# Performance work log

Hardware: AMD Instinct MI355X
Metric: run time of the kernel (lower is better)

Reference implementation:

```python
import jax, jax.numpy as jnp
import numpy as np

B, L, D, N = 4, 8192, 128, 32


def setup_inputs() -> dict:
    key = jax.random.key(0)
    ks = jax.random.split(key, 12)
    s = 0.05  # small init scale for stability of exp/cumsum
    return {
        "x": jax.random.normal(ks[0], (B, L, D), jnp.float32),
        "h_t_minus_1": jax.random.normal(ks[1], (B, L, D), jnp.float32),
        "A_log": jax.random.normal(ks[2], (D, N), jnp.float32),
        "D_param": jnp.ones((D,), jnp.float32),
        "W_x": jax.random.normal(ks[3], (D, 2 * N + D), jnp.float32) * s,
        "W_dt": jax.random.normal(ks[4], (D, D), jnp.float32) * s,
        "b_dt": jnp.zeros((D,), jnp.float32),
        "conv_w": jax.random.normal(ks[5], (3, D, D), jnp.float32) * s,  # (width, in, out)
        "conv_b": jnp.zeros((D,), jnp.float32),
        "W_f": jax.random.normal(ks[6], (D, D), jnp.float32) * s,
        "b_f": jnp.zeros((D,), jnp.float32),
    }


def reference(x, h_t_minus_1, A_log, D_param, W_x, W_dt, b_dt, conv_w, conv_b, W_f, b_f):
    d, n = A_log.shape
    A = -jnp.exp(A_log)  # (d, n)
    x_dbl = x @ W_x  # (b, l, d + 2n)
    delta, Bm, Cm = jnp.split(x_dbl, [d, d + n], axis=-1)
    delta = jax.nn.softplus(delta @ W_dt + b_dt)  # (b, l, d)

    # selective scan
    dA = jnp.einsum('bld,dn->bldn', delta, A)
    dB_u = jnp.einsum('bld,bld,bln->bldn', delta, h_t_minus_1, Bm)
    dA_cumsum = jnp.exp(jnp.cumsum(dA, axis=1) - dA)  # exclusive cumsum
    h_t = jnp.einsum('bldn,bln->bld', dB_u * dA_cumsum, Cm)
    h_t = h_t + h_t * D_param

    ssm_output = jax.nn.relu(h_t @ W_f + b_f)
    # causal Conv1D, kernel=3: left-pad by 2
    conv = jax.lax.conv_general_dilated(
        ssm_output, conv_w, window_strides=(1,), padding=[(2, 0)],
        dimension_numbers=('NWC', 'WIO', 'NWC')) + conv_b
    causal_output = jax.nn.relu(conv)
    fused_output = ssm_output * causal_output
    return (fused_output, h_t)
```

## Files before the change

### kernel.cpp

```cpp
#include <hip/hip_runtime.h>
#include <math.h>

typedef unsigned short ushort_t;
typedef __attribute__((ext_vector_type(8))) short short8v;
typedef __attribute__((ext_vector_type(4))) float f32x4;

constexpr int B_  = 4;
constexpr int L_  = 8192;
constexpr int D_  = 128;
constexpr int N_  = 32;
constexpr int BL  = B_ * L_;
constexpr int CH  = 32;
constexpr int NC  = L_ / CH;

__device__ inline unsigned bfr(float x) {
    unsigned u = __float_as_uint(x);
    return (u + 0x7fffu + ((u >> 16) & 1u)) >> 16;
}
__device__ inline unsigned pkbf(float a, float b) {
    return bfr(a) | (bfr(b) << 16);
}

__global__ __launch_bounds__(256) void prep(
    const float* __restrict__ Wx, const float* __restrict__ Wdt,
    const float* __restrict__ Wf, const float* __restrict__ Wconv,
    const float* __restrict__ A_log,
    ushort_t* __restrict__ Wt0, ushort_t* __restrict__ Wt1,
    ushort_t* __restrict__ Wt2, ushort_t* __restrict__ Wtc,
    float* __restrict__ negA)
{
    const int which = blockIdx.y;
    const int t = blockIdx.x * 256 + threadIdx.x;
    if (which == 6) {
        if (t < D_ * N_) negA[t] = -expf(A_log[t]);
        return;
    }
    const float* src; ushort_t* dst; int N;
    switch (which) {
        case 0: src = Wx;  dst = Wt0; N = 192; break;
        case 1: src = Wdt; dst = Wt1; N = 128; break;
        case 2: src = Wf;  dst = Wt2; N = 128; break;
        default:
            src = Wconv + (size_t)(which - 3) * 128 * 128;
            dst = Wtc  + (size_t)(which - 3) * 128 * 128;
            N = 128; break;
    }
    if (t >= N * 32) return;
    const int n = t >> 5, k4 = (t & 31) * 4;
    const float a0 = src[(size_t)(k4 + 0) * N + n];
    const float a1 = src[(size_t)(k4 + 1) * N + n];
    const float a2 = src[(size_t)(k4 + 2) * N + n];
    const float a3 = src[(size_t)(k4 + 3) * N + n];
    uint2 p; p.x = pkbf(a0, a1); p.y = pkbf(a2, a3);
    *reinterpret_cast<uint2*>(&dst[(size_t)n * 128 + k4]) = p;
}

template <int NCOLS, int MODE>
__global__ __launch_bounds__(256) void gemm_mfma(
    const float* __restrict__ Ag, const ushort_t* __restrict__ Wt,
    const float* __restrict__ bias,
    float* __restrict__ C0, float* __restrict__ C1, float* __restrict__ C2)
{
    __shared__ __align__(16) ushort_t Alds[64 * 64];
    __shared__ __align__(16) ushort_t Blds[NCOLS * 64];

    const int tid  = threadIdx.x;
    const int r0   = blockIdx.x * 64;
    const int wid  = tid >> 6, lane = tid & 63;
    const int wm   = wid >> 1, wn = wid & 1;
    const int lr   = lane & 15, kg = lane >> 4;
    constexpr int NF = NCOLS / 32;

    f32x4 acc[2][NF] = {};

    for (int kt = 0; kt < 128; kt += 64) {
        #pragma unroll
        for (int j = 0; j < 2; ++j) {
            const int g = tid + j * 256;
            const int row = g >> 3, k8 = (g & 7) * 8;
            const float* src = &Ag[(size_t)(r0 + row) * 128 + kt + k8];
            const float4 v0 = *reinterpret_cast<const float4*>(src);
            const float4 v1 = *reinterpret_cast<const float4*>(src + 4);
            uint4 p;
            p.x = pkbf(v0.x, v0.y); p.y = pkbf(v0.z, v0.w);
            p.z = pkbf(v1.x, v1.y); p.w = pkbf(v1.z, v1.w);
            *reinterpret_cast<uint4*>(&Alds[row * 64 + (k8 ^ ((row & 7) << 3))]) = p;
        }
        #pragma unroll
        for (int j = 0; j < NCOLS / 32; ++j) {
            const int g = tid + j * 256;
            const int n = g >> 3, k8 = (g & 7) * 8;
            const uint4 p = *reinterpret_cast<const uint4*>(&Wt[(size_t)n * 128 + kt + k8]);
            *reinterpret_cast<uint4*>(&Blds[n * 64 + (k8 ^ ((n & 7) << 3))]) = p;
        }
        __syncthreads();

        #pragma unroll
        for (int ks = 0; ks < 2; ++ks) {
            const int k8 = ks * 32 + kg * 8;
            short8v af[2];
            #pragma unroll
            for (int m = 0; m < 2; ++m) {
                const int row = wm * 32 + m * 16 + lr;
                af[m] = *reinterpret_cast<const short8v*>(
                    &Alds[row * 64 + (k8 ^ ((row & 7) << 3))]);
            }
            #pragma unroll
            for (int n = 0; n < NF; ++n) {
                const int col = wn * (NF * 16) + n * 16 + lr;
                const short8v bf = *reinterpret_cast<const short8v*>(
                    &Blds[col * 64 + (k8 ^ ((col & 7) << 3))]);
                acc[0][n] = __builtin_amdgcn_mfma_f32_16x16x32_bf16(af[0], bf, acc[0][n], 0, 0, 0);
                acc[1][n] = __builtin_amdgcn_mfma_f32_16x16x32_bf16(af[1], bf, acc[1][n], 0, 0, 0);
            }
        }
        __syncthreads();
    }

    const int fq = lane >> 4;
    #pragma unroll
    for (int m = 0; m < 2; ++m) {
        #pragma unroll
        for (int n = 0; n < NF; ++n) {
            const int col = wn * (NF * 16) + n * 16 + lr;
            #pragma unroll
            for (int q = 0; q < 4; ++q) {
                const int row = r0 + wm * 32 + m * 16 + fq * 4 + q;
                float v = acc[m][n][q];
                if (MODE == 0) {
                    if (col < 128)
                        C0[(size_t)row * 128 + col] = v;
                    else if (col < 160)
                        C1[(size_t)row * 32 + (col - 128)] = v;
                    else
                        C2[(size_t)row * 32 + (col - 160)] = v;
                } else if (MODE == 1) {
                    v += bias[col];
                    v = fmaxf(v, 0.f) + log1pf(expf(-fabsf(v)));
                    C0[(size_t)row * 128 + col] = v;
                } else {
                    C0[(size_t)row * 128 + col] = fmaxf(v + bias[col], 0.f);
                }
            }
        }
    }
}

__global__ __launch_bounds__(128) void scan_partial(
    const float* __restrict__ delta, float* __restrict__ part)
{
    const int c = blockIdx.x, b = blockIdx.y, d = threadIdx.x;
    const float* p = delta + ((size_t)b * L_ + (size_t)c * CH) * D_ + d;
    float s = 0.f;
    #pragma unroll
    for (int i = 0; i < CH; ++i) s += p[(size_t)i * D_];
    part[((size_t)b * NC + c) * D_ + d] = s;
}

__global__ __launch_bounds__(256) void scan_prefix(float* __restrict__ part)
{
    const int b = blockIdx.x, d = blockIdx.y, c = threadIdx.x;
    const int w = threadIdx.x >> 6, lane = threadIdx.x & 63;
    const size_t idx = ((size_t)b * NC + c) * D_ + d;
    const float v = part[idx];
    float s = v;
    #pragma unroll
    for (int off = 1; off < 64; off <<= 1) {
        const float t = __shfl_up(s, off, 64);
        if (lane >= off) s += t;
    }
    __shared__ float wsum[4];
    if (lane == 63) wsum[w] = s;
    __syncthreads();
    float add = 0.f;
    #pragma unroll
    for (int i = 0; i < 4; ++i)
        if (i < w) add += wsum[i];
    part[idx] = s + add - v;
}

__global__ __launch_bounds__(512) void scan_main(
    const float* __restrict__ delta, const float* __restrict__ hprev,
    const float* __restrict__ Bmat, const float* __restrict__ Cmat,
    const float* __restrict__ negA, const float* __restrict__ Dp,
    const float* __restrict__ part, float* __restrict__ h_out)
{
    __shared__ float dv_s[32][128];
    const int c = blockIdx.x, b = blockIdx.y;
    const int tid = threadIdx.x;
    const int d = tid & 127, r0 = tid >> 7;
    const int lane = tid & 63;
    const size_t rowbase = (size_t)b * L_ + (size_t)c * CH;

    #pragma unroll
    for (int j = 0; j < 2; ++j) {
        const int g = tid + j * 512;
        const int row = g >> 5, c4 = (g & 31) * 4;
        *reinterpret_cast<float4*>(&dv_s[row][c4]) =
            *reinterpret_cast<const float4*>(&delta[(rowbase + row) * D_ + c4]);
    }

    float a[N_];
    #pragma unroll
    for (int n4 = 0; n4 < 8; ++n4) {
        const float4 v = *reinterpret_cast<const float4*>(&negA[d * N_ + n4 * 4]);
        a[n4 * 4 + 0] = v.x; a[n4 * 4 + 1] = v.y;
        a[n4 * 4 + 2] = v.z; a[n4 * 4 + 3] = v.w;
    }
    const float dp1 = 1.f + Dp[d];
    __syncthreads();

    float s = part[((size_t)b * NC + c) * D_ + d];
    float sv[8];
    #pragma unroll
    for (int i = 0; i < 32; ++i) {
        if ((i & 3) == r0) sv[i >> 2] = s;
        s += dv_s[i][d];
    }

    #pragma unroll
    for (int r = 0; r < 8; ++r) {
        const int i = r * 4 + r0;
        const size_t row = rowbase + i;
        const float dv = dv_s[i][d];
        const float hv = hprev[row * D_ + d];
        const float bc = Bmat[row * N_ + (lane & 31)] * Cmat[row * N_ + (lane & 31)];
        const float sr = sv[r];
        float p0 = 0.f, p1 = 0.f, p2 = 0.f, p3 = 0.f;
        #pragma unroll
        for (int n = 0; n < N_; n += 4) {
            p0 = fmaf(__shfl(bc, n + 0), __expf(sr * a[n + 0]), p0);
            p1 = fmaf(__shfl(bc, n + 1), __expf(sr * a[n + 1]), p1);
            p2 = fmaf(__shfl(bc, n + 2), __expf(sr * a[n + 2]), p2);
            p3 = fmaf(__shfl(bc, n + 3), __expf(sr * a[n + 3]), p3);
        }
        h_out[row * D_ + d] = dv * hv * ((p0 + p1) + (p2 + p3)) * dp1;
    }
}

__global__ __launch_bounds__(256) void conv_fuse_mfma(
    const float* __restrict__ ssm, const ushort_t* __restrict__ Wtc,
    const float* __restrict__ cbias, float* __restrict__ fused)
{
    __shared__ __align__(16) ushort_t Alds[66 * 64];
    __shared__ __align__(16) ushort_t Blds[3 * 128 * 64];

    const int tid = threadIdx.x;
    const int bb = blockIdx.y;
    const int r0 = blockIdx.x * 64;
    const int wid = tid >> 6, lane = tid & 63;
    const int wm = wid >> 1, wn = wid & 1;
    const int lr = lane & 15, kg = lane >> 4;
    const float* sb = ssm + (size_t)bb * L_ * D_;

    f32x4 acc[2][4] = {};

    for (int kt = 0; kt < 128; kt += 64) {
        #pragma unroll
        for (int j = 0; j < 3; ++j) {
            const int g = tid + j * 256;
            if (g < 66 * 8) {
                const int i = g >> 3, k8 = (g & 7) * 8;
                const int gr = r0 - 2 + i;
                float4 v0 = make_float4(0.f, 0.f, 0.f, 0.f), v1 = v0;
                if (gr >= 0) {
                    const float* src = &sb[(size_t)gr * 128 + kt + k8];
                    v0 = *reinterpret_cast<const float4*>(src);
                    v1 = *reinterpret_cast<const float4*>(src + 4);
                }
                uint4 p;
                p.x = pkbf(v0.x, v0.y); p.y = pkbf(v0.z, v0.w);
                p.z = pkbf(v1.x, v1.y); p.w = pkbf(v1.z, v1.w);
                *reinterpret_cast<uint4*>(&Alds[i * 64 + (k8 ^ ((i & 7) << 3))]) = p;
            }
        }
        #pragma unroll
        for (int j = 0; j < 12; ++j) {
            const int g = tid + j * 256;
            const int row = g >> 3, k8 = (g & 7) * 8;
            const uint4 p = *reinterpret_cast<const uint4*>(&Wtc[(size_t)row * 128 + kt + k8]);
            *reinterpret_cast<uint4*>(&Blds[row * 64 + (k8 ^ ((row & 7) << 3))]) = p;
        }
        __syncthreads();

        #pragma unroll
        for (int ks = 0; ks < 2; ++ks) {
            const int k8 = ks * 32 + kg * 8;
            short8v af[2][3];
            #pragma unroll
            for (int m = 0; m < 2; ++m)
                #pragma unroll
                for (int w = 0; w < 3; ++w) {
                    const int ri = wm * 32 + m * 16 + lr + w;
                    af[m][w] = *reinterpret_cast<const short8v*>(
                        &Alds[ri * 64 + (k8 ^ ((ri & 7) << 3))]);
                }
            #pragma unroll
            for (int n = 0; n < 4; ++n) {
                const int col = wn * 64 + n * 16 + lr;
                #pragma unroll
                for (int w = 0; w < 3; ++w) {
                    const int brow = w * 128 + col;
                    const short8v bf = *reinterpret_cast<const short8v*>(
                        &Blds[brow * 64 + (k8 ^ ((brow & 7) << 3))]);
                    acc[0][n] = __builtin_amdgcn_mfma_f32_16x16x32_bf16(af[0][w], bf, acc[0][n], 0, 0, 0);
                    acc[1][n] = __builtin_amdgcn_mfma_f32_16x16x32_bf16(af[1][w], bf, acc[1][n], 0, 0, 0);
                }
            }
        }
        __syncthreads();
    }

    const int fq = lane >> 4;
    #pragma unroll
    for (int m = 0; m < 2; ++m)
        #pragma unroll
        for (int n = 0; n < 4; ++n) {
            const int col = wn * 64 + n * 16 + lr;
            #pragma unroll
            for (int q = 0; q < 4; ++q) {
                const int row = r0 + wm * 32 + m * 16 + fq * 4 + q;
                const float sv = sb[(size_t)row * 128 + col];
                const float cv = fmaxf(acc[m][n][q] + cbias[col], 0.f);
                fused[((size_t)bb * L_ + row) * 128 + col] = sv * cv;
            }
        }
}

extern "C" void kernel_launch(void* const* d_in, const int* in_sizes, int n_in,
                              void* d_out, int out_size, void* d_ws, size_t ws_size,
                              hipStream_t stream)
{
    const float* x      = (const float*)d_in[0];
    const float* hprev  = (const float*)d_in[1];
    const float* A_log  = (const float*)d_in[2];
    const float* Dp     = (const float*)d_in[3];
    const float* W_x    = (const float*)d_in[4];
    const float* W_dt   = (const float*)d_in[5];
    const float* b_dt   = (const float*)d_in[6];
    const float* conv_w = (const float*)d_in[7];
    const float* conv_b = (const float*)d_in[8];
    const float* W_f    = (const float*)d_in[9];
    const float* b_f    = (const float*)d_in[10];

    float* out   = (float*)d_out;
    float* h_out = out + (size_t)BL * D_;

    float* ws    = (float*)d_ws;
    float* draw  = ws;
    float* delta = draw + (size_t)BL * D_;
    float* Bmb   = delta + (size_t)BL * D_;
    float* Cmb   = Bmb + (size_t)BL * N_;
    float* part  = Cmb + (size_t)BL * N_;
    float* negA  = part + (size_t)B_ * NC * D_;
    ushort_t* Wt0 = (ushort_t*)(negA + D_ * N_);
    ushort_t* Wt1 = Wt0 + 192 * 128;
    ushort_t* Wt2 = Wt1 + 128 * 128;
    ushort_t* Wtc = Wt2 + 128 * 128;
    float* ssm   = draw;

    prep<<<dim3(24, 7), dim3(256), 0, stream>>>(
        W_x, W_dt, W_f, conv_w, A_log, Wt0, Wt1, Wt2, Wtc, negA);
    gemm_mfma<192, 0><<<dim3(BL / 64), dim3(256), 0, stream>>>(
        x, Wt0, nullptr, draw, Bmb, Cmb);
    gemm_mfma<128, 1><<<dim3(BL / 64), dim3(256), 0, stream>>>(
        draw, Wt1, b_dt, delta, nullptr, nullptr);
    scan_partial<<<dim3(NC, B_), dim3(128), 0, stream>>>(delta, part);
    scan_prefix<<<dim3(B_, D_), dim3(256), 0, stream>>>(part);
    scan_main<<<dim3(NC, B_), dim3(512), 0, stream>>>(
        delta, hprev, Bmb, Cmb, negA, Dp, part, h_out);
    gemm_mfma<128, 2><<<dim3(BL / 64), dim3(256), 0, stream>>>(
        h_out, Wt2, b_f, ssm, nullptr, nullptr);
    conv_fuse_mfma<<<dim3(L_ / 64, B_), dim3(256), 0, stream>>>(
        ssm, Wtc, conv_b, out);
}
```

Baseline: 181.6 us.

## Fold W_x·W_dt into one weight, fuse GEMMs into scan and conv, bf16 ssm

```diff
diff --git a/kernel.cpp b/kernel.cpp
--- a/kernel.cpp
+++ b/kernel.cpp
@@ -1,7 +1,7 @@
 #include <hip/hip_runtime.h>
 #include <math.h>
 
-typedef unsigned short ushort_t;
+typedef unsigned short u16;
 typedef __attribute__((ext_vector_type(8))) short short8v;
 typedef __attribute__((ext_vector_type(4))) float f32x4;
 
@@ -10,75 +10,72 @@
 constexpr int D_  = 128;
 constexpr int N_  = 32;
 constexpr int BL  = B_ * L_;
-constexpr int CH  = 32;
+constexpr int CH  = 16;
 constexpr int NC  = L_ / CH;
+constexpr int SCH = 32;
+constexpr int SNC = L_ / SCH;
 
 __device__ inline unsigned bfr(float x) {
     unsigned u = __float_as_uint(x);
     return (u + 0x7fffu + ((u >> 16) & 1u)) >> 16;
 }
-__device__ inline unsigned pkbf(float a, float b) {
-    return bfr(a) | (bfr(b) << 16);
-}
+__device__ inline unsigned pkbf(float a, float b) { return bfr(a) | (bfr(b) << 16); }
+__device__ inline float b2f(u16 h) { return __uint_as_float(((unsigned)h) << 16); }
 
 __global__ __launch_bounds__(256) void prep(
     const float* __restrict__ Wx, const float* __restrict__ Wdt,
     const float* __restrict__ Wf, const float* __restrict__ Wconv,
     const float* __restrict__ A_log,
-    ushort_t* __restrict__ Wt0, ushort_t* __restrict__ Wt1,
-    ushort_t* __restrict__ Wt2, ushort_t* __restrict__ Wtc,
+    u16* __restrict__ Wt0, u16* __restrict__ Wt2, u16* __restrict__ Wtc,
     float* __restrict__ negA)
 {
     const int which = blockIdx.y;
     const int t = blockIdx.x * 256 + threadIdx.x;
-    if (which == 6) {
-        if (t < D_ * N_) negA[t] = -expf(A_log[t]);
-        return;
-    }
-    const float* src; ushort_t* dst; int N;
-    switch (which) {
-        case 0: src = Wx;  dst = Wt0; N = 192; break;
-        case 1: src = Wdt; dst = Wt1; N = 128; break;
-        case 2: src = Wf;  dst = Wt2; N = 128; break;
-        default:
-            src = Wconv + (size_t)(which - 3) * 128 * 128;
-            dst = Wtc  + (size_t)(which - 3) * 128 * 128;
-            N = 128; break;
-    }
-    if (t >= N * 32) return;
-    const int n = t >> 5, k4 = (t & 31) * 4;
-    const float a0 = src[(size_t)(k4 + 0) * N + n];
-    const float a1 = src[(size_t)(k4 + 1) * N + n];
-    const float a2 = src[(size_t)(k4 + 2) * N + n];
-    const float a3 = src[(size_t)(k4 + 3) * N + n];
-    uint2 p; p.x = pkbf(a0, a1); p.y = pkbf(a2, a3);
-    *reinterpret_cast<uint2*>(&dst[(size_t)n * 128 + k4]) = p;
-}
-
-template <int NCOLS, int MODE>
-__global__ __launch_bounds__(256) void gemm_mfma(
-    const float* __restrict__ Ag, const ushort_t* __restrict__ Wt,
-    const float* __restrict__ bias,
-    float* __restrict__ C0, float* __restrict__ C1, float* __restrict__ C2)
-{
-    __shared__ __align__(16) ushort_t Alds[64 * 64];
-    __shared__ __align__(16) ushort_t Blds[NCOLS * 64];
-
-    const int tid  = threadIdx.x;
-    const int r0   = blockIdx.x * 64;
-    const int wid  = tid >> 6, lane = tid & 63;
-    const int wm   = wid >> 1, wn = wid & 1;
-    const int lr   = lane & 15, kg = lane >> 4;
-    constexpr int NF = NCOLS / 32;
-
-    f32x4 acc[2][NF] = {};
+    if (which == 0) {
+        if (t >= 128 * 128) return;
+        const int d = t >> 7, k = t & 127;
+        float s = 0.f;
+        for (int j = 0; j < 128; ++j)
+            s = fmaf(Wx[(size_t)k * 192 + j], Wdt[(size_t)j * 128 + d], s);
+        Wt0[d * 128 + k] = (u16)bfr(s);
+    } else if (which == 1) {
+        if (t >= 64 * 128) return;
+        const int n = t >> 7, k = t & 127;
+        Wt0[(128 + n) * 128 + k] = (u16)bfr(Wx[(size_t)k * 192 + 128 + n]);
+    } else if (which == 2) {
+        if (t >= 128 * 128) return;
+        const int n = t >> 7, k = t & 127;
+        Wt2[n * 128 + k] = (u16)bfr(Wf[(size_t)k * 128 + n]);
+    } else if (which <= 5) {
+        if (t >= 128 * 128) return;
+        const int w = which - 3;
+        const int n = t >> 7, k = t & 127;
+        Wtc[((size_t)w * 128 + n) * 128 + k] = (u16)bfr(Wconv[((size_t)w * 128 + k) * 128 + n]);
+    } else {
+        if (t < D_ * N_) negA[t] = -expf(A_log[t]) * 1.4426950408889634f;
+    }
+}
+
+__global__ __launch_bounds__(512) void gemm1(
+    const float* __restrict__ x, const u16* __restrict__ Wt0,
+    const float* __restrict__ b_dt,
+    float* __restrict__ delta, float* __restrict__ bc, float* __restrict__ part)
+{
+    __shared__ __align__(16) u16 Alds[64 * 64];
+    __shared__ __align__(16) u16 Blds[192 * 64];
+
+    const int tid = threadIdx.x;
+    const int r0 = blockIdx.x * 64;
+    const int wid = tid >> 6, lane = tid & 63;
+    const int wm = wid >> 1, wn = wid & 1;
+    const int lr = lane & 15, kg = lane >> 4;
+
+    f32x4 acc[6] = {};
 
     for (int kt = 0; kt < 128; kt += 64) {
-        #pragma unroll
-        for (int j = 0; j < 2; ++j) {
-            const int g = tid + j * 256;
-            const int row = g >> 3, k8 = (g & 7) * 8;
-            const float* src = &Ag[(size_t)(r0 + row) * 128 + kt + k8];
+        {
+            const int row = tid >> 3, k8 = (tid & 7) * 8;
+            const float* src = &x[(size_t)(r0 + row) * 128 + kt + k8];
             const float4 v0 = *reinterpret_cast<const float4*>(src);
             const float4 v1 = *reinterpret_cast<const float4*>(src + 4);
             uint4 p;
@@ -87,81 +84,79 @@
             *reinterpret_cast<uint4*>(&Alds[row * 64 + (k8 ^ ((row & 7) << 3))]) = p;
         }
         #pragma unroll
-        for (int j = 0; j < NCOLS / 32; ++j) {
-            const int g = tid + j * 256;
+        for (int j = 0; j < 3; ++j) {
+            const int g = tid + j * 512;
             const int n = g >> 3, k8 = (g & 7) * 8;
-            const uint4 p = *reinterpret_cast<const uint4*>(&Wt[(size_t)n * 128 + kt + k8]);
+            const uint4 p = *reinterpret_cast<const uint4*>(&Wt0[(size_t)n * 128 + kt + k8]);
             *reinterpret_cast<uint4*>(&Blds[n * 64 + (k8 ^ ((n & 7) << 3))]) = p;
         }
         __syncthreads();
-
         #pragma unroll
         for (int ks = 0; ks < 2; ++ks) {
             const int k8 = ks * 32 + kg * 8;
-            short8v af[2];
-            #pragma unroll
-            for (int m = 0; m < 2; ++m) {
-                const int row = wm * 32 + m * 16 + lr;
-                af[m] = *reinterpret_cast<const short8v*>(
-                    &Alds[row * 64 + (k8 ^ ((row & 7) << 3))]);
-            }
-            #pragma unroll
-            for (int n = 0; n < NF; ++n) {
-                const int col = wn * (NF * 16) + n * 16 + lr;
+            const int row = wm * 16 + lr;
+            const short8v af = *reinterpret_cast<const short8v*>(
+                &Alds[row * 64 + (k8 ^ ((row & 7) << 3))]);
+            #pragma unroll
+            for (int nf = 0; nf < 6; ++nf) {
+                const int col = wn * 96 + nf * 16 + lr;
                 const short8v bf = *reinterpret_cast<const short8v*>(
                     &Blds[col * 64 + (k8 ^ ((col & 7) << 3))]);
-                acc[0][n] = __builtin_amdgcn_mfma_f32_16x16x32_bf16(af[0], bf, acc[0][n], 0, 0, 0);
-                acc[1][n] = __builtin_amdgcn_mfma_f32_16x16x32_bf16(af[1], bf, acc[1][n], 0, 0, 0);
+                acc[nf] = __builtin_amdgcn_mfma_f32_16x16x32_bf16(af, bf, acc[nf], 0, 0, 0);
             }
         }
         __syncthreads();
     }
 
-    const int fq = lane >> 4;
-    #pragma unroll
-    for (int m = 0; m < 2; ++m) {
-        #pragma unroll
-        for (int n = 0; n < NF; ++n) {
-            const int col = wn * (NF * 16) + n * 16 + lr;
+    const int nDelta = wn ? 2 : 6;
+    float colsum[6];
+    #pragma unroll
+    for (int nf = 0; nf < 6; ++nf) {
+        if (nf < nDelta) {
+            const int col = wn * 96 + nf * 16 + lr;
+            const float bb = b_dt[col];
+            float s4 = 0.f;
             #pragma unroll
             for (int q = 0; q < 4; ++q) {
-                const int row = r0 + wm * 32 + m * 16 + fq * 4 + q;
-                float v = acc[m][n][q];
-                if (MODE == 0) {
-                    if (col < 128)
-                        C0[(size_t)row * 128 + col] = v;
-                    else if (col < 160)
-                        C1[(size_t)row * 32 + (col - 128)] = v;
-                    else
-                        C2[(size_t)row * 32 + (col - 160)] = v;
-                } else if (MODE == 1) {
-                    v += bias[col];
-                    v = fmaxf(v, 0.f) + log1pf(expf(-fabsf(v)));
-                    C0[(size_t)row * 128 + col] = v;
-                } else {
-                    C0[(size_t)row * 128 + col] = fmaxf(v + bias[col], 0.f);
-                }
-            }
-        }
-    }
-}
-
-__global__ __launch_bounds__(128) void scan_partial(
-    const float* __restrict__ delta, float* __restrict__ part)
-{
-    const int c = blockIdx.x, b = blockIdx.y, d = threadIdx.x;
-    const float* p = delta + ((size_t)b * L_ + (size_t)c * CH) * D_ + d;
-    float s = 0.f;
-    #pragma unroll
-    for (int i = 0; i < CH; ++i) s += p[(size_t)i * D_];
-    part[((size_t)b * NC + c) * D_ + d] = s;
-}
-
-__global__ __launch_bounds__(256) void scan_prefix(float* __restrict__ part)
-{
-    const int b = blockIdx.x, d = blockIdx.y, c = threadIdx.x;
-    const int w = threadIdx.x >> 6, lane = threadIdx.x & 63;
-    const size_t idx = ((size_t)b * NC + c) * D_ + d;
+                float v = acc[nf][q] + bb;
+                v = fmaxf(v, 0.f) + log1pf(expf(-fabsf(v)));
+                const int row = r0 + wm * 16 + kg * 4 + q;
+                delta[(size_t)row * 128 + col] = v;
+                s4 += v;
+            }
+            colsum[nf] = s4;
+        }
+    }
+    if (wn) {
+        #pragma unroll
+        for (int h = 0; h < 2; ++h)
+            #pragma unroll
+            for (int q = 0; q < 4; ++q) {
+                const int row = r0 + wm * 16 + kg * 4 + q;
+                bc[(size_t)row * 32 + h * 16 + lr] = acc[2 + h][q] * acc[4 + h][q];
+            }
+    }
+    const int b = r0 / L_;
+    const int c = (r0 % L_) / CH + wm;
+    #pragma unroll
+    for (int nf = 0; nf < 6; ++nf) {
+        if (nf < nDelta) {
+            float s = colsum[nf];
+            s += __shfl_xor(s, 16, 64);
+            s += __shfl_xor(s, 32, 64);
+            if (kg == 0) {
+                const int col = wn * 96 + nf * 16 + lr;
+                part[((size_t)b * NC + c) * 128 + col] = s;
+            }
+        }
+    }
+}
+
+__global__ __launch_bounds__(512) void scan_prefix(float* __restrict__ part)
+{
+    const int b = blockIdx.x, d = blockIdx.y;
+    const int c = threadIdx.x, w = c >> 6, lane = c & 63;
+    const size_t idx = ((size_t)b * NC + c) * 128 + d;
     const float v = part[idx];
     float s = v;
     #pragma unroll
@@ -169,37 +164,45 @@
         const float t = __shfl_up(s, off, 64);
         if (lane >= off) s += t;
     }
-    __shared__ float wsum[4];
+    __shared__ float wsum[8];
     if (lane == 63) wsum[w] = s;
     __syncthreads();
     float add = 0.f;
     #pragma unroll
-    for (int i = 0; i < 4; ++i)
+    for (int i = 0; i < 8; ++i)
         if (i < w) add += wsum[i];
     part[idx] = s + add - v;
 }
 
 __global__ __launch_bounds__(512) void scan_main(
     const float* __restrict__ delta, const float* __restrict__ hprev,
-    const float* __restrict__ Bmat, const float* __restrict__ Cmat,
-    const float* __restrict__ negA, const float* __restrict__ Dp,
-    const float* __restrict__ part, float* __restrict__ h_out)
-{
-    __shared__ float dv_s[32][128];
-    const int c = blockIdx.x, b = blockIdx.y;
+    const float* __restrict__ bc, const float* __restrict__ negA,
+    const float* __restrict__ Dp, const float* __restrict__ part,
+    const u16* __restrict__ Wt2, const float* __restrict__ b_f,
+    float* __restrict__ h_out, u16* __restrict__ ssm)
+{
+    __shared__ float delta_s[SCH][128];
+    __shared__ float bc_s[SCH][32];
+    __shared__ __align__(16) u16 h_s[SCH * 128];
+
+    const int cb = blockIdx.x, b = blockIdx.y;
     const int tid = threadIdx.x;
+    const size_t rowbase = (size_t)b * L_ + (size_t)cb * SCH;
+
+    #pragma unroll
+    for (int j = 0; j < 2; ++j) {
+        const int gg = tid + j * 512;
+        const int row = gg >> 5, c4 = (gg & 31) * 4;
+        *reinterpret_cast<float4*>(&delta_s[row][c4]) =
+            *reinterpret_cast<const float4*>(&delta[(rowbase + row) * 128 + c4]);
+    }
+    if (tid < 256) {
+        const int row = tid >> 3, c4 = (tid & 7) * 4;
+        *reinterpret_cast<float4*>(&bc_s[row][c4]) =
+            *reinterpret_cast<const float4*>(&bc[(rowbase + row) * 32 + c4]);
+    }
+
     const int d = tid & 127, r0 = tid >> 7;
-    const int lane = tid & 63;
-    const size_t rowbase = (size_t)b * L_ + (size_t)c * CH;
-
-    #pragma unroll
-    for (int j = 0; j < 2; ++j) {
-        const int g = tid + j * 512;
-        const int row = g >> 5, c4 = (g & 31) * 4;
-        *reinterpret_cast<float4*>(&dv_s[row][c4]) =
-            *reinterpret_cast<const float4*>(&delta[(rowbase + row) * D_ + c4]);
-    }
-
     float a[N_];
     #pragma unroll
     for (int n4 = 0; n4 < 8; ++n4) {
@@ -208,123 +211,139 @@
         a[n4 * 4 + 2] = v.z; a[n4 * 4 + 3] = v.w;
     }
     const float dp1 = 1.f + Dp[d];
+    float hv[8];
+    #pragma unroll
+    for (int r = 0; r < 8; ++r)
+        hv[r] = hprev[(rowbase + r * 4 + r0) * 128 + d];
+    const float sbase = part[((size_t)b * NC + cb * 2) * 128 + d];
     __syncthreads();
 
-    float s = part[((size_t)b * NC + c) * D_ + d];
     float sv[8];
-    #pragma unroll
-    for (int i = 0; i < 32; ++i) {
-        if ((i & 3) == r0) sv[i >> 2] = s;
-        s += dv_s[i][d];
-    }
-
+    {
+        float s = sbase;
+        #pragma unroll
+        for (int i = 0; i < 32; ++i) {
+            if ((i & 3) == r0) sv[i >> 2] = s;
+            s += delta_s[i][d];
+        }
+    }
     #pragma unroll
     for (int r = 0; r < 8; ++r) {
         const int i = r * 4 + r0;
-        const size_t row = rowbase + i;
-        const float dv = dv_s[i][d];
-        const float hv = hprev[row * D_ + d];
-        const float bc = Bmat[row * N_ + (lane & 31)] * Cmat[row * N_ + (lane & 31)];
+        const float dv = delta_s[i][d];
         const float sr = sv[r];
         float p0 = 0.f, p1 = 0.f, p2 = 0.f, p3 = 0.f;
         #pragma unroll
         for (int n = 0; n < N_; n += 4) {
-            p0 = fmaf(__shfl(bc, n + 0), __expf(sr * a[n + 0]), p0);
-            p1 = fmaf(__shfl(bc, n + 1), __expf(sr * a[n + 1]), p1);
-            p2 = fmaf(__shfl(bc, n + 2), __expf(sr * a[n + 2]), p2);
-            p3 = fmaf(__shfl(bc, n + 3), __expf(sr * a[n + 3]), p3);
-        }
-        h_out[row * D_ + d] = dv * hv * ((p0 + p1) + (p2 + p3)) * dp1;
-    }
-}
-
-__global__ __launch_bounds__(256) void conv_fuse_mfma(
-    const float* __restrict__ ssm, const ushort_t* __restrict__ Wtc,
+            const float4 b4 = *reinterpret_cast<const float4*>(&bc_s[i][n]);
+            p0 = fmaf(b4.x, exp2f(sr * a[n + 0]), p0);
+            p1 = fmaf(b4.y, exp2f(sr * a[n + 1]), p1);
+            p2 = fmaf(b4.z, exp2f(sr * a[n + 2]), p2);
+            p3 = fmaf(b4.w, exp2f(sr * a[n + 3]), p3);
+        }
+        const float h = dv * hv[r] * ((p0 + p1) + (p2 + p3)) * dp1;
+        h_out[(rowbase + i) * 128 + d] = h;
+        h_s[i * 128 + (((d >> 3) ^ (i & 7)) << 3) + (d & 7)] = (u16)bfr(h);
+    }
+    __syncthreads();
+
+    const int wid = tid >> 6, lane = tid & 63;
+    const int lr = lane & 15, kg = lane >> 4;
+    const int col = wid * 16 + lr;
+    f32x4 acc[2] = {};
+    #pragma unroll
+    for (int ks = 0; ks < 4; ++ks) {
+        const int k8 = ks * 32 + kg * 8;
+        const short8v bfg = *reinterpret_cast<const short8v*>(&Wt2[(size_t)col * 128 + k8]);
+        #pragma unroll
+        for (int m = 0; m < 2; ++m) {
+            const int row = m * 16 + lr;
+            const short8v afg = *reinterpret_cast<const short8v*>(
+                &h_s[row * 128 + (k8 ^ ((row & 7) << 3))]);
+            acc[m] = __builtin_amdgcn_mfma_f32_16x16x32_bf16(afg, bfg, acc[m], 0, 0, 0);
+        }
+    }
+    const float bb = b_f[col];
+    #pragma unroll
+    for (int m = 0; m < 2; ++m)
+        #pragma unroll
+        for (int q = 0; q < 4; ++q) {
+            const int row = m * 16 + kg * 4 + q;
+            const float v = fmaxf(acc[m][q] + bb, 0.f);
+            ssm[(rowbase + row) * 128 + col] = (u16)bfr(v);
+        }
+}
+
+__global__ __launch_bounds__(512) void conv_fuse(
+    const u16* __restrict__ ssm, const u16* __restrict__ Wtc,
     const float* __restrict__ cbias, float* __restrict__ fused)
 {
-    __shared__ __align__(16) ushort_t Alds[66 * 64];
-    __shared__ __align__(16) ushort_t Blds[3 * 128 * 64];
+    __shared__ __align__(16) u16 Alds[130 * 128];
 
     const int tid = threadIdx.x;
     const int bb = blockIdx.y;
-    const int r0 = blockIdx.x * 64;
+    const int r0 = blockIdx.x * 128;
+    const u16* sb = ssm + (size_t)bb * L_ * 128;
+
+    #pragma unroll
+    for (int j = 0; j < 5; ++j) {
+        const int g = tid + j * 512;
+        if (g < 130 * 16) {
+            const int i = g >> 4, k8 = (g & 15) * 8;
+            const int gr = r0 - 2 + i;
+            uint4 p = make_uint4(0, 0, 0, 0);
+            if (gr >= 0)
+                p = *reinterpret_cast<const uint4*>(&sb[(size_t)gr * 128 + k8]);
+            *reinterpret_cast<uint4*>(&Alds[i * 128 + (k8 ^ ((i & 7) << 3))]) = p;
+        }
+    }
+    __syncthreads();
+
     const int wid = tid >> 6, lane = tid & 63;
     const int wm = wid >> 1, wn = wid & 1;
     const int lr = lane & 15, kg = lane >> 4;
-    const float* sb = ssm + (size_t)bb * L_ * D_;
 
     f32x4 acc[2][4] = {};
-
-    for (int kt = 0; kt < 128; kt += 64) {
-        #pragma unroll
-        for (int j = 0; j < 3; ++j) {
-            const int g = tid + j * 256;
-            if (g < 66 * 8) {
-                const int i = g >> 3, k8 = (g & 7) * 8;
-                const int gr = r0 - 2 + i;
-                float4 v0 = make_float4(0.f, 0.f, 0.f, 0.f), v1 = v0;
-                if (gr >= 0) {
-                    const float* src = &sb[(size_t)gr * 128 + kt + k8];
-                    v0 = *reinterpret_cast<const float4*>(src);
-                    v1 = *reinterpret_cast<const float4*>(src + 4);
-                }
-                uint4 p;
-                p.x = pkbf(v0.x, v0.y); p.y = pkbf(v0.z, v0.w);
-                p.z = pkbf(v1.x, v1.y); p.w = pkbf(v1.z, v1.w);
-                *reinterpret_cast<uint4*>(&Alds[i * 64 + (k8 ^ ((i & 7) << 3))]) = p;
-            }
-        }
-        #pragma unroll
-        for (int j = 0; j < 12; ++j) {
-            const int g = tid + j * 256;
-            const int row = g >> 3, k8 = (g & 7) * 8;
-            const uint4 p = *reinterpret_cast<const uint4*>(&Wtc[(size_t)row * 128 + kt + k8]);
-            *reinterpret_cast<uint4*>(&Blds[row * 64 + (k8 ^ ((row & 7) << 3))]) = p;
-        }
-        __syncthreads();
-
-        #pragma unroll
-        for (int ks = 0; ks < 2; ++ks) {
-            const int k8 = ks * 32 + kg * 8;
-            short8v af[2][3];
-            #pragma unroll
-            for (int m = 0; m < 2; ++m)
-                #pragma unroll
-                for (int w = 0; w < 3; ++w) {
-                    const int ri = wm * 32 + m * 16 + lr + w;
-                    af[m][w] = *reinterpret_cast<const short8v*>(
-                        &Alds[ri * 64 + (k8 ^ ((ri & 7) << 3))]);
-                }
-            #pragma unroll
-            for (int n = 0; n < 4; ++n) {
-                const int col = wn * 64 + n * 16 + lr;
-                #pragma unroll
-                for (int w = 0; w < 3; ++w) {
-                    const int brow = w * 128 + col;
-                    const short8v bf = *reinterpret_cast<const short8v*>(
-                        &Blds[brow * 64 + (k8 ^ ((brow & 7) << 3))]);
-                    acc[0][n] = __builtin_amdgcn_mfma_f32_16x16x32_bf16(af[0][w], bf, acc[0][n], 0, 0, 0);
-                    acc[1][n] = __builtin_amdgcn_mfma_f32_16x16x32_bf16(af[1][w], bf, acc[1][n], 0, 0, 0);
-                }
-            }
-        }
-        __syncthreads();
-    }
-
-    const int fq = lane >> 4;
-    #pragma unroll
-    for (int m = 0; m < 2; ++m)
-        #pragma unroll
-        for (int n = 0; n < 4; ++n) {
-            const int col = wn * 64 + n * 16 + lr;
+    #pragma unroll
+    for (int ks = 0; ks < 4; ++ks) {
+        const int k8 = ks * 32 + kg * 8;
+        short8v af[2][3];
+        #pragma unroll
+        for (int m = 0; m < 2; ++m)
+            #pragma unroll
+            for (int w = 0; w < 3; ++w) {
+                const int ri = wm * 32 + m * 16 + lr + w;
+                af[m][w] = *reinterpret_cast<const short8v*>(
+                    &Alds[ri * 128 + (k8 ^ ((ri & 7) << 3))]);
+            }
+        #pragma unroll
+        for (int nf = 0; nf < 4; ++nf) {
+            const int col = wn * 64 + nf * 16 + lr;
+            #pragma unroll
+            for (int w = 0; w < 3; ++w) {
+                const short8v bfg = *reinterpret_cast<const short8v*>(
+                    &Wtc[((size_t)w * 128 + col) * 128 + k8]);
+                acc[0][nf] = __builtin_amdgcn_mfma_f32_16x16x32_bf16(af[0][w], bfg, acc[0][nf], 0, 0, 0);
+                acc[1][nf] = __builtin_amdgcn_mfma_f32_16x16x32_bf16(af[1][w], bfg, acc[1][nf], 0, 0, 0);
+            }
+        }
+    }
+
+    #pragma unroll
+    for (int nf = 0; nf < 4; ++nf) {
+        const int col = wn * 64 + nf * 16 + lr;
+        const float bb2 = cbias[col];
+        #pragma unroll
+        for (int m = 0; m < 2; ++m)
             #pragma unroll
             for (int q = 0; q < 4; ++q) {
-                const int row = r0 + wm * 32 + m * 16 + fq * 4 + q;
-                const float sv = sb[(size_t)row * 128 + col];
-                const float cv = fmaxf(acc[m][n][q] + cbias[col], 0.f);
-                fused[((size_t)bb * L_ + row) * 128 + col] = sv * cv;
-            }
-        }
+                const int row = wm * 32 + m * 16 + kg * 4 + q;
+                const int ri = row + 2;
+                const u16 sh = Alds[ri * 128 + ((((col >> 3) ^ (ri & 7)) << 3)) + (col & 7)];
+                const float cv = fmaxf(acc[m][nf][q] + bb2, 0.f);
+                fused[((size_t)bb * L_ + r0 + row) * 128 + col] = b2f(sh) * cv;
+            }
+    }
 }
 
 extern "C" void kernel_launch(void* const* d_in, const int* in_sizes, int n_in,
@@ -346,31 +365,23 @@
     float* out   = (float*)d_out;
     float* h_out = out + (size_t)BL * D_;
 
-    float* ws    = (float*)d_ws;
-    float* draw  = ws;
-    float* delta = draw + (size_t)BL * D_;
-    float* Bmb   = delta + (size_t)BL * D_;
-    float* Cmb   = Bmb + (size_t)BL * N_;
-    float* part  = Cmb + (size_t)BL * N_;
-    float* negA  = part + (size_t)B_ * NC * D_;
-    ushort_t* Wt0 = (ushort_t*)(negA + D_ * N_);
-    ushort_t* Wt1 = Wt0 + 192 * 128;
-    ushort_t* Wt2 = Wt1 + 128 * 128;
-    ushort_t* Wtc = Wt2 + 128 * 128;
-    float* ssm   = draw;
-
-    prep<<<dim3(24, 7), dim3(256), 0, stream>>>(
-        W_x, W_dt, W_f, conv_w, A_log, Wt0, Wt1, Wt2, Wtc, negA);
-    gemm_mfma<192, 0><<<dim3(BL / 64), dim3(256), 0, stream>>>(
-        x, Wt0, nullptr, draw, Bmb, Cmb);
-    gemm_mfma<128, 1><<<dim3(BL / 64), dim3(256), 0, stream>>>(
-        draw, Wt1, b_dt, delta, nullptr, nullptr);
-    scan_partial<<<dim3(NC, B_), dim3(128), 0, stream>>>(delta, part);
-    scan_prefix<<<dim3(B_, D_), dim3(256), 0, stream>>>(part);
-    scan_main<<<dim3(NC, B_), dim3(512), 0, stream>>>(
-        delta, hprev, Bmb, Cmb, negA, Dp, part, h_out);
-    gemm_mfma<128, 2><<<dim3(BL / 64), dim3(256), 0, stream>>>(
-        h_out, Wt2, b_f, ssm, nullptr, nullptr);
-    conv_fuse_mfma<<<dim3(L_ / 64, B_), dim3(256), 0, stream>>>(
+    char* ws = (char*)d_ws;
+    float* delta = (float*)ws;                  ws += (size_t)BL * 128 * 4;
+    float* bcb   = (float*)ws;                  ws += (size_t)BL * 32 * 4;
+    float* part  = (float*)ws;                  ws += (size_t)B_ * NC * 128 * 4;
+    float* negA  = (float*)ws;                  ws += (size_t)D_ * N_ * 4;
+    u16*   Wt0   = (u16*)ws;                    ws += (size_t)192 * 128 * 2;
+    u16*   Wt2   = (u16*)ws;                    ws += (size_t)128 * 128 * 2;
+    u16*   Wtc   = (u16*)ws;                    ws += (size_t)3 * 128 * 128 * 2;
+    u16*   ssm   = (u16*)ws;
+
+    prep<<<dim3(64, 7), dim3(256), 0, stream>>>(
+        W_x, W_dt, W_f, conv_w, A_log, Wt0, Wt2, Wtc, negA);
+    gemm1<<<dim3(BL / 64), dim3(512), 0, stream>>>(
+        x, Wt0, b_dt, delta, bcb, part);
+    scan_prefix<<<dim3(B_, D_), dim3(512), 0, stream>>>(part);
+    scan_main<<<dim3(SNC, B_), dim3(512), 0, stream>>>(
+        delta, hprev, bcb, negA, Dp, part, Wt2, b_f, h_out, ssm);
+    conv_fuse<<<dim3(L_ / 128, B_), dim3(512), 0, stream>>>(
         ssm, Wtc, conv_b, out);
 }
```

New measurement: 175.5 us. 1.04x faster.
